# Kernel optimization log

Hardware: AMD Instinct MI355X
Metric: run time of the kernel (lower is better)

Reference implementation:

```python
import jax, jax.numpy as jnp
import numpy as np

B, IN_F, OUT_F = 524288, 128, 128


def setup_inputs() -> dict:
    key = jax.random.key(0)
    k_x, k_wp, k_wn, k_b = jax.random.split(key, 4)
    x = jax.random.normal(k_x, (B, IN_F), dtype=jnp.float32)
    # params initialized uniform(-0.1, 0.1) as in the torch module
    weight_p = jax.random.uniform(k_wp, (OUT_F, IN_F), minval=-0.1, maxval=0.1, dtype=jnp.float32)
    weight_n = jax.random.uniform(k_wn, (OUT_F, IN_F), minval=-0.1, maxval=0.1, dtype=jnp.float32)
    bias = jax.random.uniform(k_b, (OUT_F,), minval=-0.1, maxval=0.1, dtype=jnp.float32)
    return {"x": x, "weight_p": weight_p, "weight_n": weight_n, "bias": bias}


def reference(x, weight_p, weight_n, bias):
    # ternarize: sign with >=0 -> +1 (matches torch.where(w >= 0, +1, -1))
    one = jnp.float32(1.0)
    wp = jnp.where(weight_p >= 0, one, -one)
    wn = jnp.where(weight_n >= 0, one, -one)
    # effective weight in {-1, 0, +1}
    w = (wp - wn) * jnp.float32(0.5)  # [out, in]
    out = x @ w.T + bias[None, :]      # [B, out]
    return out
```

## Files before the change

kernel.cpp:

```cpp
#include <hip/hip_runtime.h>
#include <hip/hip_bf16.h>


typedef short short8 __attribute__((ext_vector_type(8)));
typedef float f32x4 __attribute__((ext_vector_type(4)));
typedef float f32x8 __attribute__((ext_vector_type(8)));

__device__ __forceinline__ short f2bf(float f) {
  unsigned u = __builtin_bit_cast(unsigned, f);
  unsigned r = u + 0x7fffu + ((u >> 16) & 1u);
  return (short)(r >> 16);
}

__global__ void ternarize_frag_kernel(const float* __restrict__ wp,
                                      const float* __restrict__ wn,
                                      short8* __restrict__ wfrag) {
  const int tid = blockIdx.x * blockDim.x + threadIdx.x;
  const int lane = tid & 63;
  const int chunk = tid >> 6;
  const int kk = chunk >> 3, c = chunk & 7;
  const int r = lane & 15, g = lane >> 4;
  const int outcol = c * 16 + r;
  const int k0 = kk * 32 + g * 8;
  const float* p = wp + outcol * 128 + k0;
  const float* q = wn + outcol * 128 + k0;
  short8 v;
#pragma unroll
  for (int j = 0; j < 8; ++j) {
    float s = 0.5f * ((p[j] >= 0.f ? 1.f : -1.f) - (q[j] >= 0.f ? 1.f : -1.f));
    v[j] = f2bf(s);
  }
  wfrag[tid] = v;
}

__launch_bounds__(256, 2)
__global__ void stl_gemm_kernel(const float* __restrict__ x,
                                const short8* __restrict__ wfrag,
                                const float* __restrict__ bias,
                                float* __restrict__ out) {
  constexpr int IN_F = 128;
  constexpr int OUT_F = 128;
  __shared__ short8 wlds[2048];
  const int tid = threadIdx.x;
  const int wave = tid >> 6;
  const int lane = tid & 63;
  const int r = lane & 15;
  const int g = lane >> 4;
  const long row0 = (long)blockIdx.x * 128 + wave * 32;

#pragma unroll
  for (int i = 0; i < 8; ++i) {
    const int chunk = i * 256 + tid;
    __builtin_amdgcn_global_load_lds(
        (const __attribute__((address_space(1))) void*)(wfrag + chunk),
        (__attribute__((address_space(3))) void*)(wlds + chunk),
        16, 0, 0);
  }

  f32x8 xv[4][2];
#pragma unroll
  for (int kk = 0; kk < 4; ++kk)
#pragma unroll
    for (int m = 0; m < 2; ++m)
      xv[kk][m] =
          *(const f32x8*)(x + (row0 + m * 16 + r) * IN_F + kk * 32 + g * 8);
  __builtin_amdgcn_sched_barrier(0);
  __syncthreads();

  f32x4 acc[2][8] = {};
#pragma unroll
  for (int kk = 0; kk < 4; ++kk) {
    short8 bx[2];
#pragma unroll
    for (int m = 0; m < 2; ++m)
#pragma unroll
      for (int j = 0; j < 8; ++j) bx[m][j] = f2bf(xv[kk][m][j]);
#pragma unroll
    for (int c = 0; c < 8; ++c) {
      const short8 aw = wlds[(kk * 8 + c) * 64 + lane];
#pragma unroll
      for (int m = 0; m < 2; ++m)
        acc[m][c] =
            __builtin_amdgcn_mfma_f32_16x16x32_bf16(aw, bx[m], acc[m][c], 0, 0, 0);
    }
  }

#pragma unroll
  for (int c = 0; c < 8; ++c) {
    const f32x4 bv = *(const f32x4*)(bias + c * 16 + g * 4);
#pragma unroll
    for (int m = 0; m < 2; ++m) {
      f32x4 v = acc[m][c] + bv;
      *(f32x4*)(out + (row0 + m * 16 + r) * OUT_F + c * 16 + g * 4) = v;
    }
  }
}

extern "C" void kernel_launch(void* const* d_in, const int* in_sizes, int n_in,
                              void* d_out, int out_size, void* d_ws, size_t ws_size,
                              hipStream_t stream) {
  const float* x    = (const float*)d_in[0];
  const float* wp   = (const float*)d_in[1];
  const float* wn   = (const float*)d_in[2];
  const float* bias = (const float*)d_in[3];
  float* out = (float*)d_out;
  short8* wfrag = (short8*)d_ws;

  ternarize_frag_kernel<<<8, 256, 0, stream>>>(wp, wn, wfrag);

  stl_gemm_kernel<<<4096, 256, 0, stream>>>(x, wfrag, bias, out);
}
```

Measured before the change: 455.6 us.

## Make GEMM persistent per wave with double-buffered x tile prefetch

Each wave now handles 256 rows in sixteen 16-row steps instead of 32 rows once, and the grid shrinks from 4096 to 512 blocks. The weight fragments in LDS and the bias are loaded once per block and reused across all steps. The next step's x tile is loaded into a second register buffer while the current one is converted and run through MFMA, so memory latency overlaps compute. The bias also seeds the accumulators directly. The trade-off is fewer resident waves, which gives less latency hiding from occupancy, so the kernel depends more on the software prefetch keeping the memory stream busy.

```diff
diff --git a/kernel.cpp b/kernel.cpp
--- a/kernel.cpp
+++ b/kernel.cpp
@@ -38,15 +38,12 @@
                                 const short8* __restrict__ wfrag,
                                 const float* __restrict__ bias,
                                 float* __restrict__ out) {
-  constexpr int IN_F = 128;
-  constexpr int OUT_F = 128;
   __shared__ short8 wlds[2048];
   const int tid = threadIdx.x;
   const int wave = tid >> 6;
   const int lane = tid & 63;
   const int r = lane & 15;
   const int g = lane >> 4;
-  const long row0 = (long)blockIdx.x * 128 + wave * 32;
 
 #pragma unroll
   for (int i = 0; i < 8; ++i) {
@@ -57,42 +54,51 @@
         16, 0, 0);
   }
 
-  f32x8 xv[4][2];
+  f32x4 bv[8];
 #pragma unroll
-  for (int kk = 0; kk < 4; ++kk)
-#pragma unroll
-    for (int m = 0; m < 2; ++m)
-      xv[kk][m] =
-          *(const f32x8*)(x + (row0 + m * 16 + r) * IN_F + kk * 32 + g * 8);
-  __builtin_amdgcn_sched_barrier(0);
+  for (int c = 0; c < 8; ++c) bv[c] = *(const f32x4*)(bias + c * 16 + g * 4);
+
   __syncthreads();
 
-  f32x4 acc[2][8] = {};
+  const int wid = blockIdx.x * 4 + wave;
+  const long row_base = (long)wid * 256;
+  const float* xp = x + (row_base + r) * 128 + g * 8;
+  float* op = out + (row_base + r) * 128;
+
+  f32x8 xbuf[2][4];
 #pragma unroll
-  for (int kk = 0; kk < 4; ++kk) {
-    short8 bx[2];
-#pragma unroll
-    for (int m = 0; m < 2; ++m)
-#pragma unroll
-      for (int j = 0; j < 8; ++j) bx[m][j] = f2bf(xv[kk][m][j]);
-#pragma unroll
-    for (int c = 0; c < 8; ++c) {
-      const short8 aw = wlds[(kk * 8 + c) * 64 + lane];
-#pragma unroll
-      for (int m = 0; m < 2; ++m)
-        acc[m][c] =
-            __builtin_amdgcn_mfma_f32_16x16x32_bf16(aw, bx[m], acc[m][c], 0, 0, 0);
-    }
-  }
+  for (int kk = 0; kk < 4; ++kk) xbuf[0][kk] = *(const f32x8*)(xp + kk * 32);
 
 #pragma unroll
-  for (int c = 0; c < 8; ++c) {
-    const f32x4 bv = *(const f32x4*)(bias + c * 16 + g * 4);
+  for (int t = 0; t < 16; ++t) {
+    const int cur = t & 1;
+    if (t < 15) {
+      const float* xn = xp + (t + 1) * 2048;
 #pragma unroll
-    for (int m = 0; m < 2; ++m) {
-      f32x4 v = acc[m][c] + bv;
-      *(f32x4*)(out + (row0 + m * 16 + r) * OUT_F + c * 16 + g * 4) = v;
+      for (int kk = 0; kk < 4; ++kk)
+        xbuf[cur ^ 1][kk] = *(const f32x8*)(xn + kk * 32);
+      __builtin_amdgcn_sched_barrier(0);
     }
+
+    f32x4 acc[8];
+#pragma unroll
+    for (int c = 0; c < 8; ++c) acc[c] = bv[c];
+#pragma unroll
+    for (int kk = 0; kk < 4; ++kk) {
+      short8 bx;
+#pragma unroll
+      for (int j = 0; j < 8; ++j) bx[j] = f2bf(xbuf[cur][kk][j]);
+#pragma unroll
+      for (int c = 0; c < 8; ++c) {
+        const short8 aw = wlds[(kk * 8 + c) * 64 + lane];
+        acc[c] = __builtin_amdgcn_mfma_f32_16x16x32_bf16(aw, bx, acc[c], 0, 0, 0);
+      }
+    }
+
+    float* ot = op + (long)t * 2048;
+#pragma unroll
+    for (int c = 0; c < 8; ++c)
+      *(f32x4*)(ot + c * 16 + g * 4) = acc[c];
   }
 }
 
@@ -108,5 +114,5 @@
 
   ternarize_frag_kernel<<<8, 256, 0, stream>>>(wp, wn, wfrag);
 
-  stl_gemm_kernel<<<4096, 256, 0, stream>>>(x, wfrag, bias, out);
+  stl_gemm_kernel<<<512, 256, 0, stream>>>(x, wfrag, bias, out);
 }
```

New measurement: 455.8 us. Within noise of the previous version (+0.0%).
